# Kernel optimization log

Hardware: AMD Instinct MI355X
Metric: run time of the kernel (lower is better)

The kernel has to match this reference:

```python
import jax, jax.numpy as jnp
import numpy as np

B = 8192        # batch
OBS = 256       # obs_dim
ACT = 32        # action_dim -> output is 2*ACT (mu, log_std)
HID = 512       # hidden_dim
P = 8           # number of base policies (experts)
LOG_STD_MIN, LOG_STD_MAX = -5.0, 2.0


def setup_inputs() -> dict:
    key = jax.random.key(0)
    ks = jax.random.split(key, 14)
    s = 0.05
    return {
        "obs": jax.random.normal(ks[0], (B, OBS), dtype=jnp.float32),
        # gate network: obs -> HID -> HID -> P (softmax)
        "gw0": jax.random.normal(ks[1], (HID, OBS), dtype=jnp.float32) * s,
        "gb0": jnp.zeros((HID,), dtype=jnp.float32),
        "gw1": jax.random.normal(ks[2], (HID, HID), dtype=jnp.float32) * s,
        "gb1": jnp.zeros((HID,), dtype=jnp.float32),
        "gw2": jax.random.normal(ks[3], (P, HID), dtype=jnp.float32) * s,
        "gb2": jnp.zeros((P,), dtype=jnp.float32),
        # stacked expert (base-policy) trunk params, hidden_depth=2
        "ew0": jax.random.normal(ks[4], (P, HID, OBS), dtype=jnp.float32) * s,
        "eb0": jax.random.normal(ks[5], (P, HID), dtype=jnp.float32) * s,
        "ew1": jax.random.normal(ks[6], (P, HID, HID), dtype=jnp.float32) * s,
        "eb1": jax.random.normal(ks[7], (P, HID), dtype=jnp.float32) * s,
        "ew2": jax.random.normal(ks[8], (P, 2 * ACT, HID), dtype=jnp.float32) * s,
        "eb2": jax.random.normal(ks[9], (P, 2 * ACT), dtype=jnp.float32) * s,
    }


def _blend_linear(blend, W, b, x):
    # Math identical to: W_new = reshape(blend @ flatten(W,1)); bmm(W_new, x) + blend @ b
    # Contracted in the efficient order (per-expert GEMM then blend): [B,P,out] intermediate.
    y = jnp.einsum('bp,poi,bi->bo', blend, W, x, optimize=True)
    return y + blend @ b


def reference(obs, gw0, gb0, gw1, gb1, gw2, gb2, ew0, eb0, ew1, eb1, ew2, eb2):
    # gate network with softmax output
    h = jax.nn.relu(obs @ gw0.T + gb0)
    h = jax.nn.relu(h @ gw1.T + gb1)
    blend = jax.nn.softmax(h @ gw2.T + gb2, axis=-1)  # [B, P]

    # blended per-sample MLP (hidden_depth = 2)
    x = jax.nn.relu(_blend_linear(blend, ew0, eb0, obs))
    x = jax.nn.relu(_blend_linear(blend, ew1, eb1, x))
    x = _blend_linear(blend, ew2, eb2, x)  # [B, 2*ACT]

    mu, log_std = jnp.split(x, 2, axis=-1)
    log_std = jnp.tanh(log_std)
    log_std = LOG_STD_MIN + 0.5 * (LOG_STD_MAX - LOG_STD_MIN) * (log_std + 1.0)
    std = jnp.exp(log_std)
    # dist = SquashedNormal(mu, std); return its defining tensors
    return jnp.concatenate([mu, std], axis=-1)
```

## Files before the change

### kernel.cpp

```cpp
#include <hip/hip_runtime.h>
#include <hip/hip_bf16.h>
#include <cstdint>
#include <cstddef>

#define B_DIM   8192
#define OBS_DIM 256
#define ACT_DIM 32
#define HID_DIM 512
#define NEXPERT 8

typedef __attribute__((ext_vector_type(4))) float        f32x4;
typedef __attribute__((ext_vector_type(8))) short        s16x8;
typedef __attribute__((ext_vector_type(4))) unsigned int u32x4;

__device__ __forceinline__ unsigned cvt_pk_bf16(float lo, float hi) {
    unsigned r;
    asm("v_cvt_pk_bf16_f32 %0, %1, %2" : "=v"(r) : "v"(lo), "v"(hi));
    return r;
}
__device__ __forceinline__ float bf16_lo_f32(unsigned u) { return __uint_as_float(u << 16); }
__device__ __forceinline__ float bf16_hi_f32(unsigned u) { return __uint_as_float(u & 0xffff0000u); }

struct CvtArgs {
    const float*    s[7];
    unsigned short* d[7];
    int             nb[7];
};

__global__ __launch_bounds__(256) void cvt_multi(CvtArgs a) {
    int bid = blockIdx.x;
    int seg = 0, base = 0;
    while (seg < 6 && bid >= base + a.nb[seg]) { base += a.nb[seg]; ++seg; }
    int local = (bid - base) * 256 + threadIdx.x;
    const f32x4* s = (const f32x4*)a.s[seg];
    f32x4 v0 = s[local * 2 + 0];
    f32x4 v1 = s[local * 2 + 1];
    u32x4 o;
    o[0] = cvt_pk_bf16(v0[0], v0[1]);
    o[1] = cvt_pk_bf16(v0[2], v0[3]);
    o[2] = cvt_pk_bf16(v1[0], v1[1]);
    o[3] = cvt_pk_bf16(v1[2], v1[3]);
    ((u32x4*)a.d[seg])[local] = o;
}

__global__ __launch_bounds__(256) void gate_softmax(const unsigned short* __restrict__ h1,
                                                    const unsigned short* __restrict__ gw2,
                                                    const float* __restrict__ gb2,
                                                    float* __restrict__ blend) {
    const int lane = threadIdx.x & 63;
    const int wid  = threadIdx.x >> 6;
    const int row  = blockIdx.x * 4 + wid;

    u32x4 xv = *(const u32x4*)(h1 + (size_t)row * HID_DIM + lane * 8);
    float x[8];
#pragma unroll
    for (int j = 0; j < 4; ++j) {
        unsigned u   = xv[j];
        x[2 * j]     = bf16_lo_f32(u);
        x[2 * j + 1] = bf16_hi_f32(u);
    }
    float s[NEXPERT];
#pragma unroll
    for (int pp = 0; pp < NEXPERT; ++pp) {
        u32x4 wv = *(const u32x4*)(gw2 + (size_t)pp * HID_DIM + lane * 8);
        float d  = 0.f;
#pragma unroll
        for (int j = 0; j < 4; ++j) {
            unsigned u = wv[j];
            d += x[2 * j] * bf16_lo_f32(u);
            d += x[2 * j + 1] * bf16_hi_f32(u);
        }
        s[pp] = d;
    }
#pragma unroll
    for (int off = 1; off < 64; off <<= 1) {
#pragma unroll
        for (int pp = 0; pp < NEXPERT; ++pp) s[pp] += __shfl_xor(s[pp], off);
    }
    if (lane == 0) {
        float l[NEXPERT], m = -1e30f;
#pragma unroll
        for (int pp = 0; pp < NEXPERT; ++pp) { l[pp] = s[pp] + gb2[pp]; m = fmaxf(m, l[pp]); }
        float sum = 0.f;
#pragma unroll
        for (int pp = 0; pp < NEXPERT; ++pp) { l[pp] = __expf(l[pp] - m); sum += l[pp]; }
        float inv = 1.f / sum;
#pragma unroll
        for (int pp = 0; pp < NEXPERT; ++pp) blend[(size_t)row * NEXPERT + pp] = l[pp] * inv;
    }
}

template <int KIN, int NOUT>
__global__ __launch_bounds__(256, 2) void gemm_gate(const unsigned short* __restrict__ A,
                                                    const unsigned short* __restrict__ W,
                                                    const float* __restrict__ bias,
                                                    unsigned short* __restrict__ outb) {
    constexpr int BM = 128, BN = 64, BK = 64;
    constexpr int NT = KIN / BK;

    __shared__ unsigned short sA[2][BM * BK];
    __shared__ unsigned short sB[2][BN * BK];

    const int t    = threadIdx.x;
    const int lane = t & 63;
    const int wid  = t >> 6;
    const int wm   = wid >> 1, wn = wid & 1;
    const int m0   = blockIdx.x * BM;
    const int n0   = blockIdx.y * BN;

    auto stage = [&](int tile, int buf) {
        const int ks = tile * BK;
        const unsigned short* Wp = W + (size_t)n0 * KIN + ks;
#pragma unroll
        for (int c = 0; c < 2; ++c) {
            const int ch  = c * 256 + t;
            const int row = ch >> 3;
            const int gs  = (ch & 7) ^ (row & 7);
            __builtin_amdgcn_global_load_lds(
                (const __attribute__((address_space(1))) unsigned int*)(Wp + (size_t)row * KIN + gs * 8),
                (__attribute__((address_space(3))) unsigned int*)(&sB[buf][ch * 8]), 16, 0, 0);
        }
        const unsigned short* Ap = A + (size_t)m0 * KIN + ks;
#pragma unroll
        for (int c = 0; c < 4; ++c) {
            const int ch  = c * 256 + t;
            const int row = ch >> 3;
            const int gs  = (ch & 7) ^ (row & 7);
            __builtin_amdgcn_global_load_lds(
                (const __attribute__((address_space(1))) unsigned int*)(Ap + (size_t)row * KIN + gs * 8),
                (__attribute__((address_space(3))) unsigned int*)(&sA[buf][ch * 8]), 16, 0, 0);
        }
    };

    f32x4 acc[4][2];
#pragma unroll
    for (int i = 0; i < 4; ++i)
#pragma unroll
        for (int j = 0; j < 2; ++j) acc[i][j] = {0.f, 0.f, 0.f, 0.f};

    stage(0, 0);
    __syncthreads();
    int cur = 0;

#pragma unroll 1
    for (int tile = 0; tile < NT; ++tile) {
        if (tile + 1 < NT) stage(tile + 1, cur ^ 1);

#pragma unroll
        for (int kk = 0; kk < BK; kk += 32) {
            const int kb = kk + ((lane >> 4) << 3);
            s16x8 af[4], bfr[2];
#pragma unroll
            for (int mf = 0; mf < 4; ++mf) {
                const int row = wm * 64 + mf * 16 + (lane & 15);
                const int idx = (row * BK + kb) ^ ((row & 7) << 3);
                af[mf] = *(const s16x8*)(&sA[cur][idx]);
            }
#pragma unroll
            for (int nf = 0; nf < 2; ++nf) {
                const int row = wn * 32 + nf * 16 + (lane & 15);
                const int idx = (row * BK + kb) ^ ((row & 7) << 3);
                bfr[nf] = *(const s16x8*)(&sB[cur][idx]);
            }
#pragma unroll
            for (int mf = 0; mf < 4; ++mf)
#pragma unroll
                for (int nf = 0; nf < 2; ++nf)
                    acc[mf][nf] = __builtin_amdgcn_mfma_f32_16x16x32_bf16(af[mf], bfr[nf],
                                                                          acc[mf][nf], 0, 0, 0);
        }
        __syncthreads();
        cur ^= 1;
    }

    const int cn = lane & 15;
    const int rb = (lane >> 4) << 2;
#pragma unroll
    for (int nf = 0; nf < 2; ++nf) {
        const int gn   = n0 + wn * 32 + nf * 16 + cn;
        const float bv = bias[gn];
#pragma unroll
        for (int mf = 0; mf < 4; ++mf) {
#pragma unroll
            for (int r = 0; r < 4; ++r) {
                const int gm = m0 + wm * 64 + mf * 16 + rb + r;
                float v = fmaxf(acc[mf][nf][r] + bv, 0.f);
                outb[(size_t)gm * NOUT + gn] = (unsigned short)(cvt_pk_bf16(v, v) & 0xffffu);
            }
        }
    }
}

template <int KIN, int NOUT, int BN, int TPB>
__global__ __launch_bounds__(256, 2) void gemm_moe_sk(const unsigned short* __restrict__ A,
                                                      const unsigned short* __restrict__ W,
                                                      const float* __restrict__ blend,
                                                      float* __restrict__ part) {
    constexpr int BM  = 128, BK = 64;
    constexpr int NF  = BN / 32;
    constexpr int TPE = KIN / BK;
    constexpr int ET  = (TPB >= TPE) ? TPE : TPB;
    static_assert((TPB % TPE == 0) || (TPE % TPB == 0), "split/expert alignment");

    __shared__ unsigned short sA[2][BM * BK];
    __shared__ unsigned short sB[2][BN * BK];

    const int t    = threadIdx.x;
    const int lane = t & 63;
    const int wid  = t >> 6;
    const int wm   = wid >> 1, wn = wid & 1;
    const int m0   = blockIdx.x * BM;
    const int n0   = blockIdx.y * BN;
    const int sp   = blockIdx.z;

    const int cn = lane & 15;
    const int rb = (lane >> 4) << 2;
    const unsigned gbase = (unsigned)sp * TPB;

    auto stage = [&](int tile, int buf) {
        const unsigned g  = gbase + (unsigned)tile;
        const unsigned p  = g / TPE;
        const unsigned ko = (g % TPE) * BK;
        const unsigned short* Wp = W + ((size_t)p * NOUT + n0) * KIN + ko;
#pragma unroll
        for (int c = 0; c < BN / 32; ++c) {
            const int ch  = c * 256 + t;
            const int row = ch >> 3;
            const int gs  = (ch & 7) ^ (row & 7);
            __builtin_amdgcn_global_load_lds(
                (const __attribute__((address_space(1))) unsigned int*)(Wp + (size_t)row * KIN + gs * 8),
                (__attribute__((address_space(3))) unsigned int*)(&sB[buf][ch * 8]), 16, 0, 0);
        }
        const unsigned short* Ap = A + (size_t)m0 * KIN + ko;
#pragma unroll
        for (int c = 0; c < 4; ++c) {
            const int ch  = c * 256 + t;
            const int row = ch >> 3;
            const int gs  = (ch & 7) ^ (row & 7);
            __builtin_amdgcn_global_load_lds(
                (const __attribute__((address_space(1))) unsigned int*)(Ap + (size_t)row * KIN + gs * 8),
                (__attribute__((address_space(3))) unsigned int*)(&sA[buf][ch * 8]), 16, 0, 0);
        }
    };

    f32x4 mast[4][NF], eacc[4][NF];
#pragma unroll
    for (int i = 0; i < 4; ++i)
#pragma unroll
        for (int j = 0; j < NF; ++j) {
            mast[i][j] = {0.f, 0.f, 0.f, 0.f};
            eacc[i][j] = {0.f, 0.f, 0.f, 0.f};
        }

    stage(0, 0);
    __syncthreads();
    int cur = 0;

#pragma unroll 1
    for (int tile = 0; tile < TPB; ++tile) {
        if (tile + 1 < TPB) stage(tile + 1, cur ^ 1);

#pragma unroll
        for (int kk = 0; kk < BK; kk += 32) {
            const int kb = kk + ((lane >> 4) << 3);
            s16x8 af[4], bfr[NF];
#pragma unroll
            for (int mf = 0; mf < 4; ++mf) {
                const int row = wm * 64 + mf * 16 + (lane & 15);
                const int idx = (row * BK + kb) ^ ((row & 7) << 3);
                af[mf] = *(const s16x8*)(&sA[cur][idx]);
            }
#pragma unroll
            for (int nf = 0; nf < NF; ++nf) {
                const int row = wn * (BN / 2) + nf * 16 + (lane & 15);
                const int idx = (row * BK + kb) ^ ((row & 7) << 3);
                bfr[nf] = *(const s16x8*)(&sB[cur][idx]);
            }
#pragma unroll
            for (int mf = 0; mf < 4; ++mf)
#pragma unroll
                for (int nf = 0; nf < NF; ++nf)
                    eacc[mf][nf] = __builtin_amdgcn_mfma_f32_16x16x32_bf16(af[mf], bfr[nf],
                                                                           eacc[mf][nf], 0, 0, 0);
        }

        if (((tile + 1) & (ET - 1)) == 0) {
            const unsigned p = (gbase + (unsigned)tile) / TPE;
#pragma unroll
            for (int mf = 0; mf < 4; ++mf) {
#pragma unroll
                for (int r = 0; r < 4; ++r) {
                    const int gm = m0 + wm * 64 + mf * 16 + rb + r;
                    const float bl = blend[(size_t)gm * NEXPERT + p];
#pragma unroll
                    for (int nf = 0; nf < NF; ++nf) {
                        mast[mf][nf][r] += bl * eacc[mf][nf][r];
                        eacc[mf][nf][r] = 0.f;
                    }
                }
            }
        }

        __syncthreads();
        cur ^= 1;
    }

    float* dst = part + (size_t)sp * B_DIM * NOUT;
#pragma unroll
    for (int mf = 0; mf < 4; ++mf) {
#pragma unroll
        for (int r = 0; r < 4; ++r) {
            const int gm = m0 + wm * 64 + mf * 16 + rb + r;
#pragma unroll
            for (int nf = 0; nf < NF; ++nf) {
                const int gn = n0 + wn * (BN / 2) + nf * 16 + cn;
                dst[(size_t)gm * NOUT + gn] = mast[mf][nf][r];
            }
        }
    }
}

template <int NS>
__global__ __launch_bounds__(256) void reduceN_relu(const float* __restrict__ part,
                                                    const float* __restrict__ blend,
                                                    const float* __restrict__ eb,
                                                    unsigned short* __restrict__ out) {
    const int tid = blockIdx.x * 256 + threadIdx.x;
    const int row = tid >> 6;
    const int c0  = (tid & 63) << 3;

    float res[8] = {0.f, 0.f, 0.f, 0.f, 0.f, 0.f, 0.f, 0.f};
#pragma unroll
    for (int s = 0; s < NS; ++s) {
        const f32x4* ps = (const f32x4*)(part + ((size_t)s * B_DIM + row) * HID_DIM + c0);
        const f32x4 a = ps[0], b = ps[1];
#pragma unroll
        for (int j = 0; j < 4; ++j) { res[j] += a[j]; res[4 + j] += b[j]; }
    }
    const f32x4* bl = (const f32x4*)(blend + (size_t)row * NEXPERT);
    const f32x4 b0 = bl[0], b1 = bl[1];
    const float blv[8] = {b0[0], b0[1], b0[2], b0[3], b1[0], b1[1], b1[2], b1[3]};
#pragma unroll
    for (int pp = 0; pp < NEXPERT; ++pp) {
        const f32x4* e = (const f32x4*)(eb + (size_t)pp * HID_DIM + c0);
        const f32x4 e0 = e[0], e1 = e[1];
#pragma unroll
        for (int j = 0; j < 4; ++j) {
            res[j]     += blv[pp] * e0[j];
            res[4 + j] += blv[pp] * e1[j];
        }
    }
    u32x4 o;
#pragma unroll
    for (int j = 0; j < 4; ++j)
        o[j] = cvt_pk_bf16(fmaxf(res[2 * j], 0.f), fmaxf(res[2 * j + 1], 0.f));
    *(u32x4*)(out + (size_t)row * HID_DIM + c0) = o;
}

__global__ __launch_bounds__(256) void reduce8_head(const float* __restrict__ part,
                                                    const float* __restrict__ blend,
                                                    const float* __restrict__ eb2,
                                                    float* __restrict__ out) {
    const int tid = blockIdx.x * 256 + threadIdx.x;
    const int row = tid >> 3;
    const int c0  = (tid & 7) << 3;

    float res[8] = {0.f, 0.f, 0.f, 0.f, 0.f, 0.f, 0.f, 0.f};
#pragma unroll
    for (int sp = 0; sp < 8; ++sp) {
        const f32x4* ps = (const f32x4*)(part + ((size_t)sp * B_DIM + row) * 64 + c0);
        const f32x4 a = ps[0], b = ps[1];
#pragma unroll
        for (int j = 0; j < 4; ++j) { res[j] += a[j]; res[4 + j] += b[j]; }
    }
    const f32x4* bl = (const f32x4*)(blend + (size_t)row * NEXPERT);
    const f32x4 b0 = bl[0], b1 = bl[1];
    const float blv[8] = {b0[0], b0[1], b0[2], b0[3], b1[0], b1[1], b1[2], b1[3]};
#pragma unroll
    for (int pp = 0; pp < NEXPERT; ++pp) {
        const f32x4* e = (const f32x4*)(eb2 + (size_t)pp * 64 + c0);
        const f32x4 e0 = e[0], e1 = e[1];
#pragma unroll
        for (int j = 0; j < 4; ++j) {
            res[j]     += blv[pp] * e0[j];
            res[4 + j] += blv[pp] * e1[j];
        }
    }
    f32x4 o0, o1;
#pragma unroll
    for (int j = 0; j < 8; ++j) {
        const int col = c0 + j;
        float v = res[j];
        if (col >= ACT_DIM) {
            const float vc = fminf(fmaxf(v, -15.f), 15.f);
            const float e2 = __expf(2.f * vc);
            const float th = (e2 - 1.f) / (e2 + 1.f);
            v = __expf(-1.5f + 3.5f * th);
        }
        if (j < 4) o0[j] = v; else o1[j - 4] = v;
    }
    f32x4* dst = (f32x4*)(out + (size_t)row * 64 + c0);
    dst[0] = o0;
    dst[1] = o1;
}

extern "C" void kernel_launch(void* const* d_in, const int* in_sizes, int n_in,
                              void* d_out, int out_size, void* d_ws, size_t ws_size,
                              hipStream_t stream) {
    const float* obs = (const float*)d_in[0];
    const float* gw0 = (const float*)d_in[1];
    const float* gb0 = (const float*)d_in[2];
    const float* gw1 = (const float*)d_in[3];
    const float* gb1 = (const float*)d_in[4];
    const float* gw2 = (const float*)d_in[5];
    const float* gb2 = (const float*)d_in[6];
    const float* ew0 = (const float*)d_in[7];
    const float* eb0 = (const float*)d_in[8];
    const float* ew1 = (const float*)d_in[9];
    const float* eb1 = (const float*)d_in[10];
    const float* ew2 = (const float*)d_in[11];
    const float* eb2 = (const float*)d_in[12];

    char* w = (char*)d_ws;
    auto alloc = [&](size_t bytes) {
        char* r = w;
        w += (bytes + 255) & ~(size_t)255;
        return r;
    };
    unsigned short* obs_bf = (unsigned short*)alloc((size_t)B_DIM * OBS_DIM * 2);
    unsigned short* gw0_bf = (unsigned short*)alloc((size_t)HID_DIM * OBS_DIM * 2);
    unsigned short* gw1_bf = (unsigned short*)alloc((size_t)HID_DIM * HID_DIM * 2);
    unsigned short* gw2_bf = (unsigned short*)alloc((size_t)NEXPERT * HID_DIM * 2);
    unsigned short* ew0_bf = (unsigned short*)alloc((size_t)NEXPERT * HID_DIM * OBS_DIM * 2);
    unsigned short* ew1_bf = (unsigned short*)alloc((size_t)NEXPERT * HID_DIM * HID_DIM * 2);
    unsigned short* ew2_bf = (unsigned short*)alloc((size_t)NEXPERT * 2 * ACT_DIM * HID_DIM * 2);
    unsigned short* h0     = (unsigned short*)alloc((size_t)B_DIM * HID_DIM * 2);
    unsigned short* h1     = (unsigned short*)alloc((size_t)B_DIM * HID_DIM * 2);
    float*          blend  = (float*)alloc((size_t)B_DIM * NEXPERT * 4);
    float*          part   = (float*)alloc((size_t)2 * B_DIM * HID_DIM * 4);

    CvtArgs ca;
    ca.s[0] = obs; ca.d[0] = obs_bf; ca.nb[0] = (B_DIM * OBS_DIM / 8) / 256;
    ca.s[1] = gw0; ca.d[1] = gw0_bf; ca.nb[1] = (HID_DIM * OBS_DIM / 8) / 256;
    ca.s[2] = gw1; ca.d[2] = gw1_bf; ca.nb[2] = (HID_DIM * HID_DIM / 8) / 256;
    ca.s[3] = gw2; ca.d[3] = gw2_bf; ca.nb[3] = (NEXPERT * HID_DIM / 8) / 256;
    ca.s[4] = ew0; ca.d[4] = ew0_bf; ca.nb[4] = (NEXPERT * HID_DIM * OBS_DIM / 8) / 256;
    ca.s[5] = ew1; ca.d[5] = ew1_bf; ca.nb[5] = (NEXPERT * HID_DIM * HID_DIM / 8) / 256;
    ca.s[6] = ew2; ca.d[6] = ew2_bf; ca.nb[6] = (NEXPERT * 64 * HID_DIM / 8) / 256;
    int total_blocks = 0;
    for (int i = 0; i < 7; ++i) total_blocks += ca.nb[i];
    cvt_multi<<<total_blocks, 256, 0, stream>>>(ca);

    gemm_gate<OBS_DIM, HID_DIM><<<dim3(B_DIM / 128, HID_DIM / 64), 256, 0, stream>>>(
        obs_bf, gw0_bf, gb0, h0);
    gemm_gate<HID_DIM, HID_DIM><<<dim3(B_DIM / 128, HID_DIM / 64), 256, 0, stream>>>(
        h0, gw1_bf, gb1, h1);
    gate_softmax<<<B_DIM / 4, 256, 0, stream>>>(h1, gw2_bf, gb2, blend);

    gemm_moe_sk<OBS_DIM, HID_DIM, 128, 16>
        <<<dim3(B_DIM / 128, HID_DIM / 128, 2), 256, 0, stream>>>(obs_bf, ew0_bf, blend, part);
    reduceN_relu<2><<<B_DIM * 64 / 256, 256, 0, stream>>>(part, blend, eb0, h0);

    gemm_moe_sk<HID_DIM, HID_DIM, 128, 32>
        <<<dim3(B_DIM / 128, HID_DIM / 128, 2), 256, 0, stream>>>(h0, ew1_bf, blend, part);
    reduceN_relu<2><<<B_DIM * 64 / 256, 256, 0, stream>>>(part, blend, eb1, h1);

    gemm_moe_sk<HID_DIM, 64, 64, 8>
        <<<dim3(B_DIM / 128, 1, 8), 256, 0, stream>>>(h1, ew2_bf, blend, part);
    reduce8_head<<<B_DIM * 8 / 256, 256, 0, stream>>>(part, blend, eb2, (float*)d_out);
}
```

Before: 209.8 us.

## Triple-buffer MoE GEMM pipeline and fuse split-K reduce with bias+ReLU epilogue

Moves the expert GEMM from a double-buffered loop to a three-stage LDS pipeline, using explicit vmcnt waits and raw barriers in place of a full __syncthreads after each tile. Blend weights are cached in shared memory instead of being reloaded from global memory. For the two hidden layers the split-K of 2 is removed, so each block covers all experts and writes the blended bias, ReLU and bf16 output directly, which drops the fp32 partial buffers and the separate reduce kernels. The cost is half as many blocks for those layers (256 instead of 512) and more LDS per block, which may lower occupancy.

```diff
diff --git a/kernel.cpp b/kernel.cpp
--- a/kernel.cpp
+++ b/kernel.cpp
@@ -191,19 +191,24 @@
     }
 }
 
-template <int KIN, int NOUT, int BN, int TPB>
-__global__ __launch_bounds__(256, 2) void gemm_moe_sk(const unsigned short* __restrict__ A,
+template <int KIN, int NOUT, int BN, int TPB, int EPI>
+__global__ __launch_bounds__(256, 2) void gemm_moe_p3(const unsigned short* __restrict__ A,
                                                       const unsigned short* __restrict__ W,
                                                       const float* __restrict__ blend,
+                                                      const float* __restrict__ ebias,
+                                                      unsigned short* __restrict__ outb,
                                                       float* __restrict__ part) {
     constexpr int BM  = 128, BK = 64;
     constexpr int NF  = BN / 32;
     constexpr int TPE = KIN / BK;
     constexpr int ET  = (TPB >= TPE) ? TPE : TPB;
     static_assert((TPB % TPE == 0) || (TPE % TPB == 0), "split/expert alignment");
-
-    __shared__ unsigned short sA[2][BM * BK];
-    __shared__ unsigned short sB[2][BN * BK];
+    static_assert(TPB >= 4, "pipeline prologue needs >= 4 tiles");
+    static_assert(EPI == 0 || TPB == TPE, "EPI1 assumes exactly one expert/block");
+
+    __shared__ unsigned short sA[3][BM * BK];
+    __shared__ unsigned short sB[3][BN * BK];
+    __shared__ float          sBl[BM][NEXPERT];
 
     const int t    = threadIdx.x;
     const int lane = t & 63;
@@ -212,10 +217,16 @@
     const int m0   = blockIdx.x * BM;
     const int n0   = blockIdx.y * BN;
     const int sp   = blockIdx.z;
+    const unsigned gbase = (unsigned)sp * TPB;
 
     const int cn = lane & 15;
     const int rb = (lane >> 4) << 2;
-    const unsigned gbase = (unsigned)sp * TPB;
+
+    {
+        const int r = t >> 1;
+        const int c = (t & 1) * 4;
+        *(f32x4*)&sBl[r][c] = *(const f32x4*)(blend + (size_t)(m0 + r) * NEXPERT + c);
+    }
 
     auto stage = [&](int tile, int buf) {
         const unsigned g  = gbase + (unsigned)tile;
@@ -253,12 +264,29 @@
         }
 
     stage(0, 0);
+    stage(1, 1);
     __syncthreads();
+
     int cur = 0;
-
 #pragma unroll 1
     for (int tile = 0; tile < TPB; ++tile) {
-        if (tile + 1 < TPB) stage(tile + 1, cur ^ 1);
+        if (tile > 0) {
+            if (tile + 1 < TPB) {
+                if constexpr (BN == 128) {
+                    asm volatile("s_waitcnt vmcnt(8)" ::: "memory");
+                } else {
+                    asm volatile("s_waitcnt vmcnt(6)" ::: "memory");
+                }
+            } else {
+                asm volatile("s_waitcnt vmcnt(0)" ::: "memory");
+            }
+            __builtin_amdgcn_s_barrier();
+            __builtin_amdgcn_sched_barrier(0);
+        }
+        if (tile + 2 < TPB) {
+            int nb = cur + 2; if (nb >= 3) nb -= 3;
+            stage(tile + 2, nb);
+        }
 
 #pragma unroll
         for (int kk = 0; kk < BK; kk += 32) {
@@ -290,8 +318,8 @@
             for (int mf = 0; mf < 4; ++mf) {
 #pragma unroll
                 for (int r = 0; r < 4; ++r) {
-                    const int gm = m0 + wm * 64 + mf * 16 + rb + r;
-                    const float bl = blend[(size_t)gm * NEXPERT + p];
+                    const int lr = wm * 64 + mf * 16 + rb + r;
+                    const float bl = sBl[lr][p];
 #pragma unroll
                     for (int nf = 0; nf < NF; ++nf) {
                         mast[mf][nf][r] += bl * eacc[mf][nf][r];
@@ -301,60 +329,45 @@
             }
         }
 
-        __syncthreads();
-        cur ^= 1;
-    }
-
-    float* dst = part + (size_t)sp * B_DIM * NOUT;
-#pragma unroll
-    for (int mf = 0; mf < 4; ++mf) {
-#pragma unroll
-        for (int r = 0; r < 4; ++r) {
-            const int gm = m0 + wm * 64 + mf * 16 + rb + r;
-#pragma unroll
-            for (int nf = 0; nf < NF; ++nf) {
-                const int gn = n0 + wn * (BN / 2) + nf * 16 + cn;
-                dst[(size_t)gm * NOUT + gn] = mast[mf][nf][r];
-            }
-        }
-    }
-}
-
-template <int NS>
-__global__ __launch_bounds__(256) void reduceN_relu(const float* __restrict__ part,
-                                                    const float* __restrict__ blend,
-                                                    const float* __restrict__ eb,
-                                                    unsigned short* __restrict__ out) {
-    const int tid = blockIdx.x * 256 + threadIdx.x;
-    const int row = tid >> 6;
-    const int c0  = (tid & 63) << 3;
-
-    float res[8] = {0.f, 0.f, 0.f, 0.f, 0.f, 0.f, 0.f, 0.f};
-#pragma unroll
-    for (int s = 0; s < NS; ++s) {
-        const f32x4* ps = (const f32x4*)(part + ((size_t)s * B_DIM + row) * HID_DIM + c0);
-        const f32x4 a = ps[0], b = ps[1];
-#pragma unroll
-        for (int j = 0; j < 4; ++j) { res[j] += a[j]; res[4 + j] += b[j]; }
-    }
-    const f32x4* bl = (const f32x4*)(blend + (size_t)row * NEXPERT);
-    const f32x4 b0 = bl[0], b1 = bl[1];
-    const float blv[8] = {b0[0], b0[1], b0[2], b0[3], b1[0], b1[1], b1[2], b1[3]};
-#pragma unroll
-    for (int pp = 0; pp < NEXPERT; ++pp) {
-        const f32x4* e = (const f32x4*)(eb + (size_t)pp * HID_DIM + c0);
-        const f32x4 e0 = e[0], e1 = e[1];
-#pragma unroll
-        for (int j = 0; j < 4; ++j) {
-            res[j]     += blv[pp] * e0[j];
-            res[4 + j] += blv[pp] * e1[j];
-        }
-    }
-    u32x4 o;
-#pragma unroll
-    for (int j = 0; j < 4; ++j)
-        o[j] = cvt_pk_bf16(fmaxf(res[2 * j], 0.f), fmaxf(res[2 * j + 1], 0.f));
-    *(u32x4*)(out + (size_t)row * HID_DIM + c0) = o;
+        ++cur; if (cur >= 3) cur -= 3;
+    }
+
+    if constexpr (EPI == 0) {
+#pragma unroll
+        for (int nf = 0; nf < NF; ++nf) {
+            const int gn = n0 + wn * (BN / 2) + nf * 16 + cn;
+            float ebv[NEXPERT];
+#pragma unroll
+            for (int pp = 0; pp < NEXPERT; ++pp) ebv[pp] = ebias[pp * NOUT + gn];
+#pragma unroll
+            for (int mf = 0; mf < 4; ++mf) {
+#pragma unroll
+                for (int r = 0; r < 4; ++r) {
+                    const int lr = wm * 64 + mf * 16 + rb + r;
+                    float bb = 0.f;
+#pragma unroll
+                    for (int pp = 0; pp < NEXPERT; ++pp) bb += sBl[lr][pp] * ebv[pp];
+                    const float v = fmaxf(mast[mf][nf][r] + bb, 0.f);
+                    outb[(size_t)(m0 + lr) * NOUT + gn] =
+                        (unsigned short)(cvt_pk_bf16(v, v) & 0xffffu);
+                }
+            }
+        }
+    } else {
+        float* dst = part + (size_t)sp * B_DIM * NOUT;
+#pragma unroll
+        for (int mf = 0; mf < 4; ++mf) {
+#pragma unroll
+            for (int r = 0; r < 4; ++r) {
+                const int lr = wm * 64 + mf * 16 + rb + r;
+#pragma unroll
+                for (int nf = 0; nf < NF; ++nf) {
+                    const int gn = n0 + wn * (BN / 2) + nf * 16 + cn;
+                    dst[(size_t)(m0 + lr) * NOUT + gn] = mast[mf][nf][r];
+                }
+            }
+        }
+    }
 }
 
 __global__ __launch_bounds__(256) void reduce8_head(const float* __restrict__ part,
@@ -437,7 +450,7 @@
     unsigned short* h0     = (unsigned short*)alloc((size_t)B_DIM * HID_DIM * 2);
     unsigned short* h1     = (unsigned short*)alloc((size_t)B_DIM * HID_DIM * 2);
     float*          blend  = (float*)alloc((size_t)B_DIM * NEXPERT * 4);
-    float*          part   = (float*)alloc((size_t)2 * B_DIM * HID_DIM * 4);
+    float*          part   = (float*)alloc((size_t)8 * B_DIM * 64 * 4);
 
     CvtArgs ca;
     ca.s[0] = obs; ca.d[0] = obs_bf; ca.nb[0] = (B_DIM * OBS_DIM / 8) / 256;
@@ -457,15 +470,16 @@
         h0, gw1_bf, gb1, h1);
     gate_softmax<<<B_DIM / 4, 256, 0, stream>>>(h1, gw2_bf, gb2, blend);
 
-    gemm_moe_sk<OBS_DIM, HID_DIM, 128, 16>
-        <<<dim3(B_DIM / 128, HID_DIM / 128, 2), 256, 0, stream>>>(obs_bf, ew0_bf, blend, part);
-    reduceN_relu<2><<<B_DIM * 64 / 256, 256, 0, stream>>>(part, blend, eb0, h0);
-
-    gemm_moe_sk<HID_DIM, HID_DIM, 128, 32>
-        <<<dim3(B_DIM / 128, HID_DIM / 128, 2), 256, 0, stream>>>(h0, ew1_bf, blend, part);
-    reduceN_relu<2><<<B_DIM * 64 / 256, 256, 0, stream>>>(part, blend, eb1, h1);
-
-    gemm_moe_sk<HID_DIM, 64, 64, 8>
-        <<<dim3(B_DIM / 128, 1, 8), 256, 0, stream>>>(h1, ew2_bf, blend, part);
+    gemm_moe_p3<OBS_DIM, HID_DIM, 128, 32, 0>
+        <<<dim3(B_DIM / 128, HID_DIM / 128, 1), 256, 0, stream>>>(
+            obs_bf, ew0_bf, blend, eb0, h0, nullptr);
+
+    gemm_moe_p3<HID_DIM, HID_DIM, 128, 64, 0>
+        <<<dim3(B_DIM / 128, HID_DIM / 128, 1), 256, 0, stream>>>(
+            h0, ew1_bf, blend, eb1, h1, nullptr);
+
+    gemm_moe_p3<HID_DIM, 64, 64, 8, 1>
+        <<<dim3(B_DIM / 128, 1, 8), 256, 0, stream>>>(
+            h1, ew2_bf, blend, nullptr, nullptr, part);
     reduce8_head<<<B_DIM * 8 / 256, 256, 0, stream>>>(part, blend, eb2, (float*)d_out);
 }
```

Result: slower. 262.1 us (+24.9%).
